# Performance work log

Hardware: AMD Instinct MI355X
Metric: run time of the kernel (lower is better)

## Reference

```python
import jax, jax.numpy as jnp
import numpy as np

N, N1, K3, K2 = 120000, 15000, 27, 8  # points at full / stride-2 resolution, kernel volumes
C, NCLS = 32, 17

relu = jax.nn.relu

def sparse_conv(x, nbr, W):
    # gather-GEMM form of sparse 3D conv: out[m] = sum_k W[k] @ x[nbr[m,k]], nbr=-1 -> inactive offset
    valid = (nbr >= 0)[..., None].astype(x.dtype)
    g = jnp.take(x, jnp.maximum(nbr, 0), axis=0) * valid  # (M, K, Cin)
    return jnp.einsum('mkc,kco->mo', g, W)

def bnorm(x, gb, eps=1e-5):
    # batch-norm over the point dim (training-mode batch statistics); gb = [gamma; beta]
    mu = x.mean(axis=0)
    var = x.var(axis=0)
    return gb[0] * (x - mu) * jax.lax.rsqrt(var + eps) + gb[1]

def mobilevit_v2_attention(x, wi, bi, wk, bk, wv, bv, wo, bo):
    # softmax over ALL points (dim 0), global context vector, as in MobileViTv2Attention.forward
    w = jax.nn.softmax(x @ wi + bi, axis=0)                  # (M, 1)
    ctx = jnp.sum(w * (x @ wk + bk), axis=0, keepdims=True)  # (1, C)
    v = (x @ wv + bv) * ctx
    return v @ wo + bo

def setup_inputs() -> dict:
    key = jax.random.key(0)
    ks = jax.random.split(key, 30)
    f = lambda i, shape, sd: jax.random.normal(ks[i], shape, jnp.float32) * sd
    gb = lambda c: jnp.stack([jnp.ones((c,), jnp.float32), jnp.zeros((c,), jnp.float32)])
    return dict(
        x=f(0, (N, 3), 1.0),
        W_stem0=f(1, (K3, 3, C), 0.1), bn_stem0=gb(C),
        W_stem1=f(2, (K3, C, C), 0.05), bn_stem1=gb(C),
        W_down=f(3, (K2, C, C), 0.05), bn_down=gb(C),
        W_res1=f(4, (K3, C, C), 0.05), bn_res1=gb(C),
        W_res2=f(5, (K3, C, C), 0.05), bn_res2=gb(C),
        att_wi=f(6, (C, 1), 0.001), att_bi=jnp.zeros((1,), jnp.float32),
        att_wk=f(7, (C, C), 0.001), att_bk=jnp.zeros((C,), jnp.float32),
        att_wv=f(8, (C, C), 0.001), att_bv=jnp.zeros((C,), jnp.float32),
        att_wo=f(9, (C, C), 0.001), att_bo=jnp.zeros((C,), jnp.float32),
        W_up=f(10, (K2, C, C), 0.05), bn_up=gb(C),
        W_fuse1=f(11, (K3, 2 * C, C), 0.05), bn_fuse1=gb(C),
        W_fuse2=f(12, (K3, C, C), 0.05), bn_fuse2=gb(C),
        W_ds=f(13, (2 * C, C), 0.05), bn_ds=gb(C),
        W_cls=f(14, (C, NCLS), 0.05), b_cls=jnp.zeros((NCLS,), jnp.float32),
        nbr0=jax.random.randint(ks[20], (N, K3), -1, N, jnp.int32),
        nbr_down=jax.random.randint(ks[21], (N1, K2), 0, N, jnp.int32),
        nbr1=jax.random.randint(ks[22], (N1, K3), -1, N1, jnp.int32),
        nbr_up=jax.random.randint(ks[23], (N, K2), -1, N1, jnp.int32),
    )

def reference(x, W_stem0, bn_stem0, W_stem1, bn_stem1, W_down, bn_down,
              W_res1, bn_res1, W_res2, bn_res2,
              att_wi, att_bi, att_wk, att_bk, att_wv, att_bv, att_wo, att_bo,
              W_up, bn_up, W_fuse1, bn_fuse1, W_fuse2, bn_fuse2, W_ds, bn_ds,
              W_cls, b_cls, nbr0, nbr_down, nbr1, nbr_up):
    # stem: conv3+BN+ReLU x2
    x0 = relu(bnorm(sparse_conv(x, nbr0, W_stem0), bn_stem0))
    x0 = relu(bnorm(sparse_conv(x0, nbr0, W_stem1), bn_stem1))
    # stage1 downsample: BasicConvolutionBlock(ks=2, stride=2) = conv+BN+ReLU
    d = relu(bnorm(sparse_conv(x0, nbr_down, W_down), bn_down))          # (N1, C)
    # ResidualBlock with MobileViTv2 attention on the conv branch, identity shortcut
    net = bnorm(sparse_conv(relu(bnorm(sparse_conv(d, nbr1, W_res1), bn_res1)), nbr1, W_res2), bn_res2)
    net = mobilevit_v2_attention(net, att_wi, att_bi, att_wk, att_bk, att_wv, att_bv, att_wo, att_bo)
    r = relu(net + d)
    # BasicDeconvolutionBlock(ks=2, stride=2): transpose conv (gather form) + BN + ReLU
    u = relu(bnorm(sparse_conv(r, nbr_up, W_up), bn_up))                 # (N, C)
    # skip concat + ResidualBlock(2C -> C) with 1x1-conv+BN downsample shortcut
    cat = jnp.concatenate([u, x0], axis=1)                               # (N, 2C)
    net2 = bnorm(sparse_conv(relu(bnorm(sparse_conv(cat, nbr0, W_fuse1), bn_fuse1)), nbr0, W_fuse2), bn_fuse2)
    ds = bnorm(cat @ W_ds, bn_ds)
    y = relu(net2 + ds)
    # classifier
    return y @ W_cls + b_cls                                             # (N, NCLS)
```

## Files before the change

kernel.cpp:

```cpp
#include <hip/hip_runtime.h>

typedef unsigned int u32;
typedef unsigned short u16;

#define NPTS 120000
#define N1PTS 15000
#define NCLSS 17
#define NSTRIPE 16

static inline int cdiv(int a, int b) { return (a + b - 1) / b; }

typedef __attribute__((ext_vector_type(8))) short bf16x8;
typedef __attribute__((ext_vector_type(4))) float f32x4;

__device__ __forceinline__ float bflo(u32 u) { return __uint_as_float(u << 16); }
__device__ __forceinline__ float bfhi(u32 u) { return __uint_as_float(u & 0xFFFF0000u); }
__device__ __forceinline__ u32 f2bf(float f) {
    u32 u = __float_as_uint(f);
    return (u + 0x7FFFu + ((u >> 16) & 1u)) >> 16;
}
__device__ __forceinline__ u32 pack2(float a, float b) { return f2bf(a) | (f2bf(b) << 16); }

__device__ __forceinline__ f32x4 mfma16(bf16x8 a, uint4 b, f32x4 c) {
    return __builtin_amdgcn_mfma_f32_16x16x32_bf16(a, __builtin_bit_cast(bf16x8, b), c, 0, 0, 0);
}

template<int K>
__global__ __launch_bounds__(256) void transpose_nbr(
    const int* __restrict__ nbr, int* __restrict__ nbrT, int M)
{
    __shared__ int tile[256][K + 1];
    int p0 = blockIdx.x * 256;
    int t = threadIdx.x;
    int np = M - p0; if (np > 256) np = 256;
    int total = np * K;
    for (int i = t; i < total; i += 256) {
        int lp = i / K, k = i - lp * K;
        tile[lp][k] = nbr[(size_t)p0 * K + i];
    }
    __syncthreads();
    if (t < np) {
#pragma unroll
        for (int k = 0; k < K; ++k)
            nbrT[(size_t)k * M + p0 + t] = tile[t][k];
    }
}

struct WbArgs {
    const float* src[8];
    uint4* dst[8];
    int CINF[8];
    int COFF[8];
    int K2[8];
};

__global__ __launch_bounds__(64) void convert_wb(WbArgs a) {
    int j = blockIdx.y;
    int s2 = blockIdx.x;
    if (s2 >= a.K2[j]) return;
    int lane = threadIdx.x;
    int k = s2 >> 1, tile = s2 & 1;
    int c = a.COFF[j] + (lane >> 4) * 8;
    int o = tile * 16 + (lane & 15);
    const float* w = a.src[j] + ((size_t)k * a.CINF[j] + c) * 32 + o;
    u32 hw[4], lw[4];
#pragma unroll
    for (int q = 0; q < 4; ++q) {
        float w0 = w[(2 * q) * 32], w1 = w[(2 * q + 1) * 32];
        u32 h0 = f2bf(w0), h1 = f2bf(w1);
        float r0 = w0 - __uint_as_float(h0 << 16);
        float r1 = w1 - __uint_as_float(h1 << 16);
        hw[q] = h0 | (h1 << 16);
        lw[q] = f2bf(r0) | (f2bf(r1) << 16);
    }
    uint4 hv; hv.x = hw[0]; hv.y = hw[1]; hv.z = hw[2]; hv.w = hw[3];
    uint4 lv; lv.x = lw[0]; lv.y = lw[1]; lv.z = lw[2]; lv.w = lw[3];
    a.dst[j][(size_t)(s2 * 2 + 0) * 64 + lane] = hv;
    a.dst[j][(size_t)(s2 * 2 + 1) * 64 + lane] = lv;
}

template<int KB, int MODE, int NPH>
__global__ __launch_bounds__(1024, 8) void conv_part(
    const u16* __restrict__ src, const int* __restrict__ nbrTk,
    const uint4* __restrict__ wb, float* __restrict__ T,
    u16* __restrict__ out, float* __restrict__ stats, int M, int Msrc)
{
    __shared__ uint4 wl[KB * 256];
    __shared__ int il[KB * 256];
    __shared__ float red[15][64];
    int tid = threadIdx.x;
    int lane = tid & 63, wid = tid >> 6;
    int p0 = blockIdx.x * 256 + wid * 16;
    int row = lane & 15, hi4 = lane >> 4;
    int lpt = wid * 16 + row;
    int col = lane & 15;
    const uint4 z4 = {0u, 0u, 0u, 0u};

    for (int i = tid; i < KB * 256; i += 1024) wl[i] = wb[i];
    for (int i = tid; i < KB * 256; i += 1024) {
        int k = i >> 8, pl = i & 255;
        int pp = blockIdx.x * 256 + pl;
        il[i] = (pp < M) ? nbrTk[(size_t)k * M + pp] : -1;
    }

    f32x4 acc0, acc1;
    if (MODE >= 1) {
#pragma unroll
        for (int r = 0; r < 4; ++r) {
            int pp = p0 + hi4 * 4 + r;
            int ps = pp < M ? pp : 0;
            acc0[r] = T[(size_t)ps * 32 + col];
            acc1[r] = T[(size_t)ps * 32 + 16 + col];
        }
    } else {
        acc0 = {0.f, 0.f, 0.f, 0.f};
        acc1 = {0.f, 0.f, 0.f, 0.f};
    }

    __syncthreads();

    const int PHSZ = (Msrc + NPH - 1) / NPH;

    auto gld = [&](int k, int lo, int hi) -> uint4 {
        int idx = il[(k << 8) + lpt];
        uint4 r = z4;
        if (idx >= lo && idx < hi)
            r = reinterpret_cast<const uint4*>(src + (size_t)idx * 32)[hi4];
        return r;
    };

#pragma unroll 1
    for (int ph = 0; ph < NPH; ++ph) {
        int lo = (NPH == 1) ? 0 : ph * PHSZ;
        int hi = (NPH == 1) ? 0x7FFFFFFF : lo + PHSZ;
        uint4 g0 = gld(0, lo, hi);
        uint4 g1 = (KB > 1) ? gld(1, lo, hi) : z4;
        uint4 g2 = (KB > 2) ? gld(2, lo, hi) : z4;
#pragma unroll 1
        for (int k = 0; k < KB; ++k) {
            uint4 gn = (k + 3 < KB) ? gld(k + 3, lo, hi) : z4;
            const uint4* bl = &wl[k * 256];
            bf16x8 a = __builtin_bit_cast(bf16x8, g0);
            acc0 = mfma16(a, bl[lane], acc0);
            acc0 = mfma16(a, bl[64 + lane], acc0);
            acc1 = mfma16(a, bl[128 + lane], acc1);
            acc1 = mfma16(a, bl[192 + lane], acc1);
            g0 = g1; g1 = g2; g2 = gn;
        }
    }

    if (MODE <= 1) {
#pragma unroll
        for (int r = 0; r < 4; ++r) {
            int pp = p0 + hi4 * 4 + r;
            if (pp < M) {
                T[(size_t)pp * 32 + col] = acc0[r];
                T[(size_t)pp * 32 + 16 + col] = acc1[r];
            }
        }
        return;
    }

#pragma unroll
    for (int r = 0; r < 4; ++r) {
        int pp = p0 + hi4 * 4 + r;
        if (pp < M) {
            out[(size_t)pp * 32 + col] = (u16)f2bf(acc0[r]);
            out[(size_t)pp * 32 + 16 + col] = (u16)f2bf(acc1[r]);
        }
    }
    float s0 = 0.f, q0 = 0.f, s1 = 0.f, q1 = 0.f;
#pragma unroll
    for (int r = 0; r < 4; ++r) {
        s0 += acc0[r]; q0 += acc0[r] * acc0[r];
        s1 += acc1[r]; q1 += acc1[r] * acc1[r];
    }
#pragma unroll
    for (int m = 16; m <= 32; m <<= 1) {
        s0 += __shfl_xor(s0, m, 64); q0 += __shfl_xor(q0, m, 64);
        s1 += __shfl_xor(s1, m, 64); q1 += __shfl_xor(q1, m, 64);
    }
    float val = (lane < 16) ? s0 : (lane < 32) ? s1 : (lane < 48) ? q0 : q1;
    if (wid > 0) red[wid - 1][lane] = val;
    __syncthreads();
    if (wid == 0) {
        float t = val;
#pragma unroll
        for (int w = 0; w < 15; ++w) t += red[w][lane];
        atomicAdd(&stats[((blockIdx.x & (NSTRIPE - 1)) << 6) + lane], t);
    }
}

__global__ __launch_bounds__(1024, 8) void conv_blk8(
    const u16* __restrict__ src, const int* __restrict__ nbrT,
    const uint4* __restrict__ wb, u16* __restrict__ out,
    float* __restrict__ stats, int M)
{
    constexpr int K = 8;
    __shared__ uint4 wl[K * 256];
    __shared__ int il[K * 256];
    __shared__ float red[15][64];
    int tid = threadIdx.x;
    int lane = tid & 63, wid = tid >> 6;
    int p0 = blockIdx.x * 256 + wid * 16;
    int row = lane & 15, hi4 = lane >> 4;
    int lpt = wid * 16 + row;
    const uint4 z4 = {0u, 0u, 0u, 0u};

    for (int i = tid; i < K * 256; i += 1024) wl[i] = wb[i];
    for (int i = tid; i < K * 256; i += 1024) {
        int k = i >> 8, pl = i & 255;
        int pp = blockIdx.x * 256 + pl;
        il[i] = (pp < M) ? nbrT[(size_t)k * M + pp] : -1;
    }

    f32x4 acc0 = {0.f, 0.f, 0.f, 0.f};
    f32x4 acc1 = {0.f, 0.f, 0.f, 0.f};

    __syncthreads();

    auto gld = [&](int k) -> uint4 {
        int idx = il[(k << 8) + lpt];
        int j = idx >= 0 ? idx : 0;
        uint4 v = reinterpret_cast<const uint4*>(src + (size_t)j * 32)[hi4];
        u32 m = (idx >= 0) ? 0xFFFFFFFFu : 0u;
        uint4 r; r.x = v.x & m; r.y = v.y & m; r.z = v.z & m; r.w = v.w & m;
        return r;
    };

    uint4 g0 = gld(0);
    uint4 g1 = gld(1);
    uint4 g2 = gld(2);

#pragma unroll 1
    for (int k = 0; k < K; ++k) {
        uint4 gn = (k + 3 < K) ? gld(k + 3) : z4;
        const uint4* bl = &wl[k * 256];
        bf16x8 a = __builtin_bit_cast(bf16x8, g0);
        acc0 = mfma16(a, bl[lane], acc0);
        acc0 = mfma16(a, bl[64 + lane], acc0);
        acc1 = mfma16(a, bl[128 + lane], acc1);
        acc1 = mfma16(a, bl[192 + lane], acc1);
        g0 = g1; g1 = g2; g2 = gn;
    }

#pragma unroll
    for (int r = 0; r < 4; ++r) {
        int pp = p0 + hi4 * 4 + r;
        if (pp < M) {
            out[(size_t)pp * 32 + (lane & 15)] = (u16)f2bf(acc0[r]);
            out[(size_t)pp * 32 + 16 + (lane & 15)] = (u16)f2bf(acc1[r]);
        }
    }

    float s0 = 0.f, q0 = 0.f, s1 = 0.f, q1 = 0.f;
#pragma unroll
    for (int r = 0; r < 4; ++r) {
        s0 += acc0[r]; q0 += acc0[r] * acc0[r];
        s1 += acc1[r]; q1 += acc1[r] * acc1[r];
    }
#pragma unroll
    for (int m = 16; m <= 32; m <<= 1) {
        s0 += __shfl_xor(s0, m, 64); q0 += __shfl_xor(q0, m, 64);
        s1 += __shfl_xor(s1, m, 64); q1 += __shfl_xor(q1, m, 64);
    }
    float val = (lane < 16) ? s0 : (lane < 32) ? s1 : (lane < 48) ? q0 : q1;
    if (wid > 0) red[wid - 1][lane] = val;
    __syncthreads();
    if (wid == 0) {
        float t = val;
#pragma unroll
        for (int w = 0; w < 15; ++w) t += red[w][lane];
        atomicAdd(&stats[((blockIdx.x & (NSTRIPE - 1)) << 6) + lane], t);
    }
}

template<int K>
__global__ __launch_bounds__(256, 6) void conv_mfma(
    const u16* __restrict__ src, const int* __restrict__ nbrT,
    const uint4* __restrict__ wb, u16* __restrict__ out,
    float* __restrict__ stats, int M)
{
    constexpr int KS = K;
    constexpr int NCH = (KS + 1) / 2;
    __shared__ uint4 wlds[2][512];
    __shared__ float red[4][64];

    int tid = threadIdx.x;
    int lane = tid & 63, wid = tid >> 6;
    int p0 = blockIdx.x * 64 + wid * 16;
    int row = lane & 15, hi4 = lane >> 4;
    int p = p0 + row;
    bool rowok = p < M;
    const uint4 z4 = {0u, 0u, 0u, 0u};

    f32x4 acc0 = {0.f, 0.f, 0.f, 0.f};
    f32x4 acc1 = {0.f, 0.f, 0.f, 0.f};

    {
        uint4 a0 = wb[tid], a1 = wb[256 + tid];
        wlds[0][tid] = a0; wlds[0][256 + tid] = a1;
    }
    uint4 av0 = z4, av1 = z4;
    {
        int iA = -1, iB = -1;
        if (rowok) {
            iA = nbrT[p];
            if (KS > 1) iB = nbrT[(size_t)M + p];
        }
        if (iA >= 0) av0 = reinterpret_cast<const uint4*>(src + (size_t)iA * 32)[hi4];
        if (KS > 1 && iB >= 0) av1 = reinterpret_cast<const uint4*>(src + (size_t)iB * 32)[hi4];
    }

    uint4 wr0 = z4, wr1 = z4;
#pragma unroll 1
    for (int c = 0; c < NCH; ++c) {
        bool last = (c + 1 >= NCH);
        if (!last) {
            wr0 = wb[(size_t)(c + 1) * 512 + tid];
            wr1 = wb[(size_t)(c + 1) * 512 + 256 + tid];
        }
        int nA = -1, nB = -1;
        if (!last && rowok) {
            int s0 = 2 * c + 2;
            nA = nbrT[(size_t)s0 * M + p];
            if (s0 + 1 < KS) nB = nbrT[(size_t)(s0 + 1) * M + p];
        }
        asm volatile("s_waitcnt lgkmcnt(0)" ::: "memory");
        __builtin_amdgcn_s_barrier();
        asm volatile("" ::: "memory");
        uint4 nav0 = z4, nav1 = z4;
        if (nA >= 0) nav0 = reinterpret_cast<const uint4*>(src + (size_t)nA * 32)[hi4];
        if (nB >= 0) nav1 = reinterpret_cast<const uint4*>(src + (size_t)nB * 32)[hi4];

        const uint4* bl = wlds[c & 1];
        {
            bf16x8 a = __builtin_bit_cast(bf16x8, av0);
            acc0 = mfma16(a, bl[lane], acc0);
            acc0 = mfma16(a, bl[64 + lane], acc0);
            acc1 = mfma16(a, bl[128 + lane], acc1);
            acc1 = mfma16(a, bl[192 + lane], acc1);
        }
        if (2 * c + 1 < KS) {
            bf16x8 a = __builtin_bit_cast(bf16x8, av1);
            acc0 = mfma16(a, bl[256 + lane], acc0);
            acc0 = mfma16(a, bl[320 + lane], acc0);
            acc1 = mfma16(a, bl[384 + lane], acc1);
            acc1 = mfma16(a, bl[448 + lane], acc1);
        }
        if (!last) {
            wlds[(c + 1) & 1][tid] = wr0;
            wlds[(c + 1) & 1][256 + tid] = wr1;
        }
        av0 = nav0; av1 = nav1;
    }

#pragma unroll
    for (int r = 0; r < 4; ++r) {
        int pp = p0 + hi4 * 4 + r;
        if (pp < M) {
            out[(size_t)pp * 32 + (lane & 15)] = (u16)f2bf(acc0[r]);
            out[(size_t)pp * 32 + 16 + (lane & 15)] = (u16)f2bf(acc1[r]);
        }
    }

    float s0 = 0.f, q0 = 0.f, s1 = 0.f, q1 = 0.f;
#pragma unroll
    for (int r = 0; r < 4; ++r) {
        s0 += acc0[r]; q0 += acc0[r] * acc0[r];
        s1 += acc1[r]; q1 += acc1[r] * acc1[r];
    }
#pragma unroll
    for (int m = 16; m <= 32; m <<= 1) {
        s0 += __shfl_xor(s0, m, 64); q0 += __shfl_xor(q0, m, 64);
        s1 += __shfl_xor(s1, m, 64); q1 += __shfl_xor(q1, m, 64);
    }
    float val = (lane < 16) ? s0 : (lane < 32) ? s1 : (lane < 48) ? q0 : q1;
    red[wid][lane] = val;
    __syncthreads();
    if (wid == 0) {
        float t = red[0][lane] + red[1][lane] + red[2][lane] + red[3][lane];
        atomicAdd(&stats[((blockIdx.x & (NSTRIPE - 1)) << 6) + lane], t);
    }
}

__device__ __forceinline__ void reduce_store_stats(
    float (&acc)[32], int lane, int wid, bool act, int p,
    u16* __restrict__ out, float* __restrict__ sst)
{
    __shared__ float lds[3][64][17];
#pragma unroll
    for (int r = 0; r < 2; ++r) {
        if (wid > 0) {
#pragma unroll
            for (int j = 0; j < 16; ++j) lds[wid - 1][lane][j] = acc[r * 16 + j];
        }
        __syncthreads();
        if (wid == 0) {
#pragma unroll
            for (int w = 0; w < 3; ++w)
#pragma unroll
                for (int j = 0; j < 16; ++j) acc[r * 16 + j] += lds[w][lane][j];
        }
        __syncthreads();
    }
    if (wid == 0) {
        if (act) {
            u32 wd[16];
#pragma unroll
            for (int q = 0; q < 16; ++q) wd[q] = pack2(acc[2 * q], acc[2 * q + 1]);
            uint4* dst = reinterpret_cast<uint4*>(out + (size_t)p * 32);
            uint4 v;
            v.x = wd[0];  v.y = wd[1];  v.z = wd[2];  v.w = wd[3];  dst[0] = v;
            v.x = wd[4];  v.y = wd[5];  v.z = wd[6];  v.w = wd[7];  dst[1] = v;
            v.x = wd[8];  v.y = wd[9];  v.z = wd[10]; v.w = wd[11]; dst[2] = v;
            v.x = wd[12]; v.y = wd[13]; v.z = wd[14]; v.w = wd[15]; dst[3] = v;
        } else {
#pragma unroll
            for (int o = 0; o < 32; ++o) acc[o] = 0.f;
        }
        float sel1 = 0.f, sel2 = 0.f;
#pragma unroll
        for (int o = 0; o < 32; ++o) {
            float s1 = acc[o], s2 = acc[o] * acc[o];
#pragma unroll
            for (int m = 1; m <= 32; m <<= 1) { s1 += __shfl_xor(s1, m, 64); s2 += __shfl_xor(s2, m, 64); }
            if (lane == o) sel1 = s1;
            if (lane == o + 32) sel2 = s2;
        }
        atomicAdd(&sst[lane], lane < 32 ? sel1 : sel2);
    }
}

__global__ __launch_bounds__(256, 8) void conv_x3(
    const float* __restrict__ src, const int* __restrict__ nbrT,
    const float* __restrict__ W, u16* __restrict__ out,
    float* __restrict__ stats, int M)
{
    constexpr int K = 27;
    int lane = threadIdx.x & 63;
    int wid = __builtin_amdgcn_readfirstlane(threadIdx.x >> 6);
    int p = blockIdx.x * 64 + lane;
    bool act = p < M;
    constexpr int JMAX = 7;

    float acc[32];
#pragma unroll
    for (int o = 0; o < 32; ++o) acc[o] = 0.f;

    int idxs[JMAX];
#pragma unroll
    for (int j = 0; j < JMAX; ++j) {
        int k = wid + 4 * j;
        idxs[j] = (act && k < K) ? nbrT[(size_t)k * M + p] : -1;
    }
#pragma unroll
    for (int j = 0; j < JMAX; ++j) {
        int k = wid + 4 * j;
        if (k >= K) break;
        int idx = idxs[j];
        if (idx >= 0) {
            const float* __restrict__ xr = src + (size_t)idx * 3;
            const float* __restrict__ wk = W + (size_t)k * 3 * 32;
            float x0 = xr[0], x1 = xr[1], x2 = xr[2];
#pragma unroll
            for (int o = 0; o < 32; ++o) {
                float s = fmaf(x0, wk[o], 0.f);
                s = fmaf(x1, wk[32 + o], s);
                acc[o] += fmaf(x2, wk[64 + o], s);
            }
        }
    }
    reduce_store_stats(acc, lane, wid, act, p, out,
                       stats + ((blockIdx.x & (NSTRIPE - 1)) << 6));
}

__global__ __launch_bounds__(256, 4) void conv_ds2(
    const u16* __restrict__ u, const u16* __restrict__ x0,
    const float* __restrict__ W, u16* __restrict__ out,
    float* __restrict__ stats, int M)
{
    int lane = threadIdx.x & 63;
    int wid = __builtin_amdgcn_readfirstlane(threadIdx.x >> 6);
    int p = blockIdx.x * 64 + lane;
    bool act = p < M;

    float acc[32];
#pragma unroll
    for (int o = 0; o < 32; ++o) acc[o] = 0.f;

    if (act) {
        const u16* srcp = (wid < 2) ? u : x0;
        const uint4* xr = reinterpret_cast<const uint4*>(srcp + (size_t)p * 32 + (wid & 1) * 16);
        const float* wk = W + (size_t)wid * 16 * 32;
#pragma unroll
        for (int h = 0; h < 2; ++h) {
            uint4 v = xr[h];
            float xv[8] = { bflo(v.x), bfhi(v.x), bflo(v.y), bfhi(v.y),
                            bflo(v.z), bfhi(v.z), bflo(v.w), bfhi(v.w) };
#pragma unroll
            for (int c = 0; c < 8; ++c)
#pragma unroll
                for (int o = 0; o < 32; ++o)
                    acc[o] = fmaf(xv[c], wk[(h * 8 + c) * 32 + o], acc[o]);
        }
    }
    reduce_store_stats(acc, lane, wid, act, p, out,
                       stats + ((blockIdx.x & (NSTRIPE - 1)) << 6));
}

template<bool RELU>
__global__ __launch_bounds__(256) void bn_apply(
    u16* __restrict__ buf, const float* __restrict__ stats,
    const float* __restrict__ gb, float invM, int total)
{
    __shared__ float ab[64];
    if (threadIdx.x < 32) {
        int c = threadIdx.x;
        float s = 0.f, q = 0.f;
#pragma unroll
        for (int st = 0; st < NSTRIPE; ++st) {
            s += stats[st * 64 + c];
            q += stats[st * 64 + 32 + c];
        }
        float mu = s * invM;
        float var = fmaxf(q * invM - mu * mu, 0.f);
        float a = gb[c] * rsqrtf(var + 1e-5f);
        ab[c] = a;
        ab[32 + c] = gb[32 + c] - mu * a;
    }
    __syncthreads();
    int i = blockIdx.x * 256 + threadIdx.x;
    if (i >= total) return;
    int c0 = (i & 3) * 8;
    uint4 v = reinterpret_cast<uint4*>(buf)[i];
    u32 w[4] = { v.x, v.y, v.z, v.w };
    u32 r[4];
#pragma unroll
    for (int q = 0; q < 4; ++q) {
        int c = c0 + 2 * q;
        float y0 = fmaf(ab[c], bflo(w[q]), ab[32 + c]);
        float y1 = fmaf(ab[c + 1], bfhi(w[q]), ab[32 + c + 1]);
        if (RELU) { y0 = fmaxf(y0, 0.f); y1 = fmaxf(y1, 0.f); }
        r[q] = pack2(y0, y1);
    }
    uint4 o; o.x = r[0]; o.y = r[1]; o.z = r[2]; o.w = r[3];
    reinterpret_cast<uint4*>(buf)[i] = o;
}

__device__ __forceinline__ void load_row32(const u16* __restrict__ base, int p, float (&nv)[32])
{
    const uint4* xr = reinterpret_cast<const uint4*>(base + (size_t)p * 32);
#pragma unroll
    for (int q = 0; q < 4; ++q) {
        uint4 v = xr[q];
        nv[q * 8 + 0] = bflo(v.x); nv[q * 8 + 1] = bfhi(v.x);
        nv[q * 8 + 2] = bflo(v.y); nv[q * 8 + 3] = bfhi(v.y);
        nv[q * 8 + 4] = bflo(v.z); nv[q * 8 + 5] = bfhi(v.z);
        nv[q * 8 + 6] = bflo(v.w); nv[q * 8 + 7] = bfhi(v.w);
    }
}

__global__ __launch_bounds__(256) void att_logits(
    const u16* __restrict__ net, const float* __restrict__ wi,
    const float* __restrict__ bi, float* __restrict__ lbuf,
    u32* __restrict__ mx, int M)
{
    int p = blockIdx.x * 256 + threadIdx.x;
    float l = -3.0e38f;
    if (p < M) {
        float nv[32];
        load_row32(net, p, nv);
        float s = bi[0];
#pragma unroll
        for (int c = 0; c < 32; ++c) s = fmaf(nv[c], wi[c], s);
        lbuf[p] = s;
        l = s;
    }
#pragma unroll
    for (int m = 1; m <= 32; m <<= 1) l = fmaxf(l, __shfl_xor(l, m, 64));
    if ((threadIdx.x & 63) == 0) {
        u32 b = __float_as_uint(l);
        u32 e = (b & 0x80000000u) ? ~b : (b | 0x80000000u);
        atomicMax(mx, e);
    }
}

__global__ __launch_bounds__(256) void att_accum(
    const u16* __restrict__ net, const float* __restrict__ lbuf,
    float* __restrict__ att, int M)
{
    int p = blockIdx.x * 256 + threadIdx.x;
    int lane = threadIdx.x & 63, wid = threadIdx.x >> 6;
    u32 um = __float_as_uint(att[0]);
    float mx = (um & 0x80000000u) ? __uint_as_float(um ^ 0x80000000u) : __uint_as_float(~um);
    float w = 0.f;
    float nv[32];
#pragma unroll
    for (int c = 0; c < 32; ++c) nv[c] = 0.f;
    if (p < M) {
        w = expf(lbuf[p] - mx);
        load_row32(net, p, nv);
    }
    float sel = 0.f;
#pragma unroll
    for (int c = 0; c < 32; ++c) {
        float s = w * nv[c];
#pragma unroll
        for (int m = 1; m <= 32; m <<= 1) s += __shfl_xor(s, m, 64);
        if (lane == c) sel = s;
    }
    {
        float s = w;
#pragma unroll
        for (int m = 1; m <= 32; m <<= 1) s += __shfl_xor(s, m, 64);
        if (lane == 32) sel = s;
    }
    __shared__ float red[4][33];
    if (lane < 33) red[wid][lane] = sel;
    __syncthreads();
    if (wid == 0 && lane < 33) {
        float t = red[0][lane] + red[1][lane] + red[2][lane] + red[3][lane];
        atomicAdd(lane < 32 ? &att[2 + lane] : &att[1], t);
    }
}

__global__ void att_ctx_k(const float* __restrict__ wk, const float* __restrict__ bk,
                          float* __restrict__ att)
{
    int o = threadIdx.x;
    if (o >= 32) return;
    float invS = 1.0f / att[1];
    float s = bk[o];
#pragma unroll
    for (int c = 0; c < 32; ++c) s = fmaf(att[2 + c] * invS, wk[c * 32 + o], s);
    att[34 + o] = s;
}

__global__ __launch_bounds__(256) void att_out_res(
    const u16* __restrict__ net, const u16* __restrict__ d,
    const float* __restrict__ wv, const float* __restrict__ bv,
    const float* __restrict__ wo, const float* __restrict__ bo,
    const float* __restrict__ att, u16* __restrict__ r, int M)
{
    int p = blockIdx.x * 256 + threadIdx.x;
    if (p >= M) return;
    float nv[32];
    load_row32(net, p, nv);
    float vv[32];
#pragma unroll
    for (int o = 0; o < 32; ++o) {
        float s = bv[o];
#pragma unroll
        for (int c = 0; c < 32; ++c) s = fmaf(nv[c], wv[c * 32 + o], s);
        vv[o] = s * att[34 + o];
    }
    float dv[32];
    load_row32(d, p, dv);
    u32 wd[16];
#pragma unroll
    for (int q = 0; q < 16; ++q) {
        float y[2];
#pragma unroll
        for (int t = 0; t < 2; ++t) {
            int oo = 2 * q + t;
            float s = bo[oo];
#pragma unroll
            for (int o = 0; o < 32; ++o) s = fmaf(vv[o], wo[o * 32 + oo], s);
            y[t] = fmaxf(s + dv[oo], 0.f);
        }
        wd[q] = pack2(y[0], y[1]);
    }
    uint4* dst = reinterpret_cast<uint4*>(r + (size_t)p * 32);
    uint4 v;
    v.x = wd[0];  v.y = wd[1];  v.z = wd[2];  v.w = wd[3];  dst[0] = v;
    v.x = wd[4];  v.y = wd[5];  v.z = wd[6];  v.w = wd[7];  dst[1] = v;
    v.x = wd[8];  v.y = wd[9];  v.z = wd[10]; v.w = wd[11]; dst[2] = v;
    v.x = wd[12]; v.y = wd[13]; v.z = wd[14]; v.w = wd[15]; dst[3] = v;
}

__global__ __launch_bounds__(256) void final_cls(
    const u16* __restrict__ net2, const u16* __restrict__ dsr,
    const float* __restrict__ st7, const float* __restrict__ st8,
    const float* __restrict__ gb7, const float* __restrict__ gb8,
    const float* __restrict__ wcls, const float* __restrict__ bcls,
    float* __restrict__ outp, float invM, int M)
{
    __shared__ float ab7[64], ab8[64];
    if (threadIdx.x < 64) {
        int c = threadIdx.x & 31;
        const float* st = (threadIdx.x < 32) ? st7 : st8;
        const float* g  = (threadIdx.x < 32) ? gb7 : gb8;
        float* abp      = (threadIdx.x < 32) ? ab7 : ab8;
        float s = 0.f, q = 0.f;
#pragma unroll
        for (int k = 0; k < NSTRIPE; ++k) {
            s += st[k * 64 + c];
            q += st[k * 64 + 32 + c];
        }
        float mu = s * invM;
        float var = fmaxf(q * invM - mu * mu, 0.f);
        float a = g[c] * rsqrtf(var + 1e-5f);
        abp[c] = a;
        abp[32 + c] = g[32 + c] - mu * a;
    }
    __syncthreads();
    int p = blockIdx.x * 256 + threadIdx.x;
    if (p >= M) return;
    float nv[32], dv[32];
    load_row32(net2, p, nv);
    load_row32(dsr, p, dv);
    float y[32];
#pragma unroll
    for (int c = 0; c < 32; ++c) {
        float t = fmaf(ab7[c], nv[c], ab7[32 + c]) + fmaf(ab8[c], dv[c], ab8[32 + c]);
        y[c] = fmaxf(t, 0.f);
    }
#pragma unroll
    for (int j = 0; j < NCLSS; ++j) {
        float s = bcls[j];
#pragma unroll
        for (int c = 0; c < 32; ++c) s = fmaf(y[c], wcls[c * NCLSS + j], s);
        outp[(size_t)p * NCLSS + j] = s;
    }
}

extern "C" void kernel_launch(void* const* d_in, const int* in_sizes, int n_in,
                              void* d_out, int out_size, void* d_ws, size_t ws_size,
                              hipStream_t stream)
{
    char* wsb = (char*)d_ws;

    float* ST  = (float*)wsb;
    float* ATT = ST + 9216;
    float* L   = (float*)(wsb + 65536);
    const size_t SZN = 7680000ull;
    const size_t SZ1 = 960000ull;
    u16* A  = (u16*)(wsb + 131072);
    u16* B  = (u16*)(wsb + 131072 + SZN);
    u16* C  = (u16*)(wsb + 131072 + 2 * SZN);
    u16* D  = (u16*)(wsb + 131072 + 2 * SZN + SZ1);
    u16* E  = (u16*)(wsb + 131072 + 2 * SZN + 2 * SZ1);
    u16* G  = (u16*)(wsb + 131072 + 2 * SZN + 3 * SZ1);
    float* T = (float*)(wsb + 131072 + 3 * SZN + 3 * SZ1);

    size_t wboff = 131072 + 3 * SZN + 3 * SZ1 + 15360000ull;
    auto wbsz = [](int K) { return (size_t)((K + 1) & ~1) * 4096; };
    uint4* wb_stem1 = (uint4*)(wsb + wboff);         size_t o1 = wboff + wbsz(27);
    uint4* wb_down  = (uint4*)(wsb + o1);            size_t o2 = o1 + wbsz(8);
    uint4* wb_res1  = (uint4*)(wsb + o2);            size_t o3 = o2 + wbsz(27);
    uint4* wb_res2  = (uint4*)(wsb + o3);            size_t o4 = o3 + wbsz(27);
    uint4* wb_up    = (uint4*)(wsb + o4);            size_t o5 = o4 + wbsz(8);
    uint4* wb_f1A   = (uint4*)(wsb + o5);            size_t o6 = o5 + wbsz(27);
    uint4* wb_f1B   = (uint4*)(wsb + o6);            size_t o7 = o6 + wbsz(27);
    uint4* wb_fuse2 = (uint4*)(wsb + o7);            size_t o8 = o7 + wbsz(27);

    int* nbrT0 = (int*)(wsb + o8);                   size_t o9  = o8 + 27ull * NPTS * 4;
    int* nbrTd = (int*)(wsb + o9);                   size_t o10 = o9 + 8ull * N1PTS * 4;
    int* nbrT1 = (int*)(wsb + o10);                  size_t o11 = o10 + 27ull * N1PTS * 4;
    int* nbrTu = (int*)(wsb + o11);

    const float* X        = (const float*)d_in[0];
    const float* Wstem0   = (const float*)d_in[1];
    const float* gb_stem0 = (const float*)d_in[2];
    const float* Wstem1   = (const float*)d_in[3];
    const float* gb_stem1 = (const float*)d_in[4];
    const float* Wdown    = (const float*)d_in[5];
    const float* gb_down  = (const float*)d_in[6];
    const float* Wres1    = (const float*)d_in[7];
    const float* gb_res1  = (const float*)d_in[8];
    const float* Wres2    = (const float*)d_in[9];
    const float* gb_res2  = (const float*)d_in[10];
    const float* wi = (const float*)d_in[11];
    const float* bi = (const float*)d_in[12];
    const float* wk = (const float*)d_in[13];
    const float* bk = (const float*)d_in[14];
    const float* wv = (const float*)d_in[15];
    const float* bv = (const float*)d_in[16];
    const float* wo = (const float*)d_in[17];
    const float* bo = (const float*)d_in[18];
    const float* Wup      = (const float*)d_in[19];
    const float* gb_up    = (const float*)d_in[20];
    const float* Wfuse1   = (const float*)d_in[21];
    const float* gb_fuse1 = (const float*)d_in[22];
    const float* Wfuse2   = (const float*)d_in[23];
    const float* gb_fuse2 = (const float*)d_in[24];
    const float* Wds      = (const float*)d_in[25];
    const float* gb_ds    = (const float*)d_in[26];
    const float* Wcls     = (const float*)d_in[27];
    const float* bcls     = (const float*)d_in[28];

    const int* nbr0     = (const int*)d_in[29];
    const int* nbr_down = (const int*)d_in[30];
    const int* nbr1     = (const int*)d_in[31];
    const int* nbr_up   = (const int*)d_in[32];

    const float invN  = 1.0f / (float)NPTS;
    const float invN1 = 1.0f / (float)N1PTS;

    hipMemsetAsync((void*)ST, 0, (9216 + 66) * sizeof(float), stream);

    hipLaunchKernelGGL((transpose_nbr<27>), dim3(cdiv(NPTS, 256)), dim3(256), 0, stream,
                       nbr0, nbrT0, NPTS);
    hipLaunchKernelGGL((transpose_nbr<8>), dim3(cdiv(N1PTS, 256)), dim3(256), 0, stream,
                       nbr_down, nbrTd, N1PTS);
    hipLaunchKernelGGL((transpose_nbr<27>), dim3(cdiv(N1PTS, 256)), dim3(256), 0, stream,
                       nbr1, nbrT1, N1PTS);
    hipLaunchKernelGGL((transpose_nbr<8>), dim3(cdiv(NPTS, 256)), dim3(256), 0, stream,
                       nbr_up, nbrTu, NPTS);

    {
        WbArgs a;
        a.src[0] = Wstem1; a.dst[0] = wb_stem1; a.CINF[0] = 32; a.COFF[0] = 0;  a.K2[0] = 54;
        a.src[1] = Wdown;  a.dst[1] = wb_down;  a.CINF[1] = 32; a.COFF[1] = 0;  a.K2[1] = 16;
        a.src[2] = Wres1;  a.dst[2] = wb_res1;  a.CINF[2] = 32; a.COFF[2] = 0;  a.K2[2] = 54;
        a.src[3] = Wres2;  a.dst[3] = wb_res2;  a.CINF[3] = 32; a.COFF[3] = 0;  a.K2[3] = 54;
        a.src[4] = Wup;    a.dst[4] = wb_up;    a.CINF[4] = 32; a.COFF[4] = 0;  a.K2[4] = 16;
        a.src[5] = Wfuse1; a.dst[5] = wb_f1A;   a.CINF[5] = 64; a.COFF[5] = 0;  a.K2[5] = 54;
        a.src[6] = Wfuse1; a.dst[6] = wb_f1B;   a.CINF[6] = 64; a.COFF[6] = 32; a.K2[6] = 54;
        a.src[7] = Wfuse2; a.dst[7] = wb_fuse2; a.CINF[7] = 32; a.COFF[7] = 0;  a.K2[7] = 54;
        hipLaunchKernelGGL(convert_wb, dim3(54, 8), dim3(64), 0, stream, a);
    }

    const int gS   = cdiv(NPTS, 64);
    const int gB   = cdiv(NPTS, 256);
    const int gM1  = cdiv(N1PTS, 64);
    const int gBN  = cdiv(NPTS * 4, 256);
    const int gBN1 = cdiv(N1PTS * 4, 256);
    const int gN1p = cdiv(N1PTS, 256);
    const int gN   = cdiv(NPTS, 256);
    const int KH0 = 14;

    hipLaunchKernelGGL(conv_x3, dim3(gS), dim3(256), 0, stream,
                       X, nbrT0, Wstem0, A, ST + 0 * 1024, NPTS);
    hipLaunchKernelGGL((bn_apply<true>), dim3(gBN), dim3(256), 0, stream,
                       A, ST + 0 * 1024, gb_stem0, invN, NPTS * 4);
    hipLaunchKernelGGL((conv_part<14, 0, 2>), dim3(gB), dim3(1024), 0, stream,
                       A, nbrT0, wb_stem1, T, (u16*)nullptr, (float*)nullptr, NPTS, NPTS);
    hipLaunchKernelGGL((conv_part<13, 2, 2>), dim3(gB), dim3(1024), 0, stream,
                       A, nbrT0 + (size_t)KH0 * NPTS, wb_stem1 + KH0 * 256, T, B, ST + 1 * 1024, NPTS, NPTS);
    hipLaunchKernelGGL((bn_apply<true>), dim3(gBN), dim3(256), 0, stream,
                       B, ST + 1 * 1024, gb_stem1, invN, NPTS * 4);

    hipLaunchKernelGGL((conv_mfma<8>), dim3(gM1), dim3(256), 0, stream,
                       B, nbrTd, wb_down, C, ST + 2 * 1024, N1PTS);
    hipLaunchKernelGGL((bn_apply<true>), dim3(gBN1), dim3(256), 0, stream,
                       C, ST + 2 * 1024, gb_down, invN1, N1PTS * 4);

    hipLaunchKernelGGL((conv_mfma<27>), dim3(gM1), dim3(256), 0, stream,
                       C, nbrT1, wb_res1, D, ST + 3 * 1024, N1PTS);
    hipLaunchKernelGGL((bn_apply<true>), dim3(gBN1), dim3(256), 0, stream,
                       D, ST + 3 * 1024, gb_res1, invN1, N1PTS * 4);
    hipLaunchKernelGGL((conv_mfma<27>), dim3(gM1), dim3(256), 0, stream,
                       D, nbrT1, wb_res2, E, ST + 4 * 1024, N1PTS);
    hipLaunchKernelGGL((bn_apply<false>), dim3(gBN1), dim3(256), 0, stream,
                       E, ST + 4 * 1024, gb_res2, invN1, N1PTS * 4);

    hipLaunchKernelGGL(att_logits, dim3(gN1p), dim3(256), 0, stream,
                       E, wi, bi, L, (u32*)ATT, N1PTS);
    hipLaunchKernelGGL(att_accum, dim3(gN1p), dim3(256), 0, stream, E, L, ATT, N1PTS);
    hipLaunchKernelGGL(att_ctx_k, dim3(1), dim3(64), 0, stream, wk, bk, ATT);
    hipLaunchKernelGGL(att_out_res, dim3(gN1p), dim3(256), 0, stream,
                       E, C, wv, bv, wo, bo, ATT, D, N1PTS);

    hipLaunchKernelGGL(conv_blk8, dim3(gB), dim3(1024), 0, stream,
                       D, nbrTu, wb_up, A, ST + 5 * 1024, NPTS);
    hipLaunchKernelGGL((bn_apply<true>), dim3(gBN), dim3(256), 0, stream,
                       A, ST + 5 * 1024, gb_up, invN, NPTS * 4);

    hipLaunchKernelGGL((conv_part<14, 0, 2>), dim3(gB), dim3(1024), 0, stream,
                       A, nbrT0, wb_f1A, T, (u16*)nullptr, (float*)nullptr, NPTS, NPTS);
    hipLaunchKernelGGL((conv_part<13, 1, 2>), dim3(gB), dim3(1024), 0, stream,
                       A, nbrT0 + (size_t)KH0 * NPTS, wb_f1A + KH0 * 256, T,
                       (u16*)nullptr, (float*)nullptr, NPTS, NPTS);
    hipLaunchKernelGGL((conv_part<14, 1, 2>), dim3(gB), dim3(1024), 0, stream,
                       B, nbrT0, wb_f1B, T, (u16*)nullptr, (float*)nullptr, NPTS, NPTS);
    hipLaunchKernelGGL(conv_ds2, dim3(gS), dim3(256), 0, stream,
                       A, B, Wds, G, ST + 8 * 1024, NPTS);
    hipLaunchKernelGGL((conv_part<13, 2, 2>), dim3(gB), dim3(1024), 0, stream,
                       B, nbrT0 + (size_t)KH0 * NPTS, wb_f1B + KH0 * 256, T, A, ST + 6 * 1024, NPTS, NPTS);
    hipLaunchKernelGGL((bn_apply<true>), dim3(gBN), dim3(256), 0, stream,
                       A, ST + 6 * 1024, gb_fuse1, invN, NPTS * 4);

    hipLaunchKernelGGL((conv_part<14, 0, 2>), dim3(gB), dim3(1024), 0, stream,
                       A, nbrT0, wb_fuse2, T, (u16*)nullptr, (float*)nullptr, NPTS, NPTS);
    hipLaunchKernelGGL((conv_part<13, 2, 2>), dim3(gB), dim3(1024), 0, stream,
                       A, nbrT0 + (size_t)KH0 * NPTS, wb_fuse2 + KH0 * 256, T, B, ST + 7 * 1024, NPTS, NPTS);

    hipLaunchKernelGGL(final_cls, dim3(gN), dim3(256), 0, stream,
                       B, G, ST + 7 * 1024, ST + 8 * 1024, gb_fuse2, gb_ds,
                       Wcls, bcls, (float*)d_out, invN, NPTS);
}
```

Before: 375.4 us.

## Fuse BN+ReLU apply into consumer conv gathers, drop standalone bn_apply passes

Result: slower. 528.4 us (+40.7%).

```diff
diff --git a/kernel.cpp b/kernel.cpp
--- a/kernel.cpp
+++ b/kernel.cpp
@@ -20,9 +20,27 @@
     return (u + 0x7FFFu + ((u >> 16) & 1u)) >> 16;
 }
 __device__ __forceinline__ u32 pack2(float a, float b) { return f2bf(a) | (f2bf(b) << 16); }
+__device__ __forceinline__ float bfround(float f) { return __uint_as_float(f2bf(f) << 16); }
 
 __device__ __forceinline__ f32x4 mfma16(bf16x8 a, uint4 b, f32x4 c) {
     return __builtin_amdgcn_mfma_f32_16x16x32_bf16(a, __builtin_bit_cast(bf16x8, b), c, 0, 0, 0);
+}
+
+__device__ __forceinline__ void stats_to_ab(
+    const float* __restrict__ bst, const float* __restrict__ bgb,
+    float binvM, int c, float* __restrict__ abl)
+{
+    float s = 0.f, q = 0.f;
+#pragma unroll
+    for (int st = 0; st < NSTRIPE; ++st) {
+        s += bst[st * 64 + c];
+        q += bst[st * 64 + 32 + c];
+    }
+    float mu = s * binvM;
+    float var = fmaxf(q * binvM - mu * mu, 0.f);
+    float a = bgb[c] * rsqrtf(var + 1e-5f);
+    abl[c] = a;
+    abl[32 + c] = bgb[32 + c] - mu * a;
 }
 
 template<int K>
@@ -79,15 +97,18 @@
     a.dst[j][(size_t)(s2 * 2 + 1) * 64 + lane] = lv;
 }
 
-template<int KB, int MODE, int NPH>
+template<int KB, int MODE, int NPH, bool BN>
 __global__ __launch_bounds__(1024, 8) void conv_part(
     const u16* __restrict__ src, const int* __restrict__ nbrTk,
     const uint4* __restrict__ wb, float* __restrict__ T,
-    u16* __restrict__ out, float* __restrict__ stats, int M, int Msrc)
+    u16* __restrict__ out, float* __restrict__ stats,
+    const float* __restrict__ bst, const float* __restrict__ bgb, float binvM,
+    int M, int Msrc)
 {
     __shared__ uint4 wl[KB * 256];
     __shared__ int il[KB * 256];
     __shared__ float red[15][64];
+    __shared__ float abl[64];
     int tid = threadIdx.x;
     int lane = tid & 63, wid = tid >> 6;
     int p0 = blockIdx.x * 256 + wid * 16;
@@ -96,6 +117,8 @@
     int col = lane & 15;
     const uint4 z4 = {0u, 0u, 0u, 0u};
 
+    if (BN && tid < 32) stats_to_ab(bst, bgb, binvM, tid, abl);
+
     for (int i = tid; i < KB * 256; i += 1024) wl[i] = wb[i];
     for (int i = tid; i < KB * 256; i += 1024) {
         int k = i >> 8, pl = i & 255;
@@ -119,13 +142,31 @@
 
     __syncthreads();
 
+    float la[8], lb[8];
+    if (BN) {
+#pragma unroll
+        for (int j = 0; j < 8; ++j) { la[j] = abl[hi4 * 8 + j]; lb[j] = abl[32 + hi4 * 8 + j]; }
+    }
+
     const int PHSZ = (Msrc + NPH - 1) / NPH;
 
     auto gld = [&](int k, int lo, int hi) -> uint4 {
         int idx = il[(k << 8) + lpt];
         uint4 r = z4;
-        if (idx >= lo && idx < hi)
-            r = reinterpret_cast<const uint4*>(src + (size_t)idx * 32)[hi4];
+        if (idx >= lo && idx < hi) {
+            uint4 v = reinterpret_cast<const uint4*>(src + (size_t)idx * 32)[hi4];
+            if (BN) {
+                u32 w[4] = { v.x, v.y, v.z, v.w };
+#pragma unroll
+                for (int q2 = 0; q2 < 4; ++q2) {
+                    float y0 = fmaxf(fmaf(la[2 * q2], bflo(w[q2]), lb[2 * q2]), 0.f);
+                    float y1 = fmaxf(fmaf(la[2 * q2 + 1], bfhi(w[q2]), lb[2 * q2 + 1]), 0.f);
+                    w[q2] = pack2(y0, y1);
+                }
+                v.x = w[0]; v.y = w[1]; v.z = w[2]; v.w = w[3];
+            }
+            r = v;
+        }
         return r;
     };
 
@@ -275,16 +316,19 @@
     }
 }
 
-template<int K>
+template<int K, bool BN>
 __global__ __launch_bounds__(256, 6) void conv_mfma(
     const u16* __restrict__ src, const int* __restrict__ nbrT,
     const uint4* __restrict__ wb, u16* __restrict__ out,
-    float* __restrict__ stats, int M)
+    float* __restrict__ stats,
+    const float* __restrict__ bst, const float* __restrict__ bgb, float binvM,
+    int M)
 {
     constexpr int KS = K;
     constexpr int NCH = (KS + 1) / 2;
     __shared__ uint4 wlds[2][512];
     __shared__ float red[4][64];
+    __shared__ float abl[64];
 
     int tid = threadIdx.x;
     int lane = tid & 63, wid = tid >> 6;
@@ -297,10 +341,31 @@
     f32x4 acc0 = {0.f, 0.f, 0.f, 0.f};
     f32x4 acc1 = {0.f, 0.f, 0.f, 0.f};
 
+    if (BN && tid < 32) stats_to_ab(bst, bgb, binvM, tid, abl);
     {
         uint4 a0 = wb[tid], a1 = wb[256 + tid];
         wlds[0][tid] = a0; wlds[0][256 + tid] = a1;
     }
+    __syncthreads();
+
+    float la[8], lb[8];
+    if (BN) {
+#pragma unroll
+        for (int j = 0; j < 8; ++j) { la[j] = abl[hi4 * 8 + j]; lb[j] = abl[32 + hi4 * 8 + j]; }
+    }
+    auto bnfix = [&](uint4 v) -> uint4 {
+        if (!BN) return v;
+        u32 w[4] = { v.x, v.y, v.z, v.w };
+#pragma unroll
+        for (int q2 = 0; q2 < 4; ++q2) {
+            float y0 = fmaxf(fmaf(la[2 * q2], bflo(w[q2]), lb[2 * q2]), 0.f);
+            float y1 = fmaxf(fmaf(la[2 * q2 + 1], bfhi(w[q2]), lb[2 * q2 + 1]), 0.f);
+            w[q2] = pack2(y0, y1);
+        }
+        uint4 r2; r2.x = w[0]; r2.y = w[1]; r2.z = w[2]; r2.w = w[3];
+        return r2;
+    };
+
     uint4 av0 = z4, av1 = z4;
     {
         int iA = -1, iB = -1;
@@ -308,8 +373,8 @@
             iA = nbrT[p];
             if (KS > 1) iB = nbrT[(size_t)M + p];
         }
-        if (iA >= 0) av0 = reinterpret_cast<const uint4*>(src + (size_t)iA * 32)[hi4];
-        if (KS > 1 && iB >= 0) av1 = reinterpret_cast<const uint4*>(src + (size_t)iB * 32)[hi4];
+        if (iA >= 0) av0 = bnfix(reinterpret_cast<const uint4*>(src + (size_t)iA * 32)[hi4]);
+        if (KS > 1 && iB >= 0) av1 = bnfix(reinterpret_cast<const uint4*>(src + (size_t)iB * 32)[hi4]);
     }
 
     uint4 wr0 = z4, wr1 = z4;
@@ -330,8 +395,8 @@
         __builtin_amdgcn_s_barrier();
         asm volatile("" ::: "memory");
         uint4 nav0 = z4, nav1 = z4;
-        if (nA >= 0) nav0 = reinterpret_cast<const uint4*>(src + (size_t)nA * 32)[hi4];
-        if (nB >= 0) nav1 = reinterpret_cast<const uint4*>(src + (size_t)nB * 32)[hi4];
+        if (nA >= 0) nav0 = bnfix(reinterpret_cast<const uint4*>(src + (size_t)nA * 32)[hi4]);
+        if (nB >= 0) nav1 = bnfix(reinterpret_cast<const uint4*>(src + (size_t)nB * 32)[hi4]);
 
         const uint4* bl = wlds[c & 1];
         {
@@ -478,16 +543,35 @@
 __global__ __launch_bounds__(256, 4) void conv_ds2(
     const u16* __restrict__ u, const u16* __restrict__ x0,
     const float* __restrict__ W, u16* __restrict__ out,
-    float* __restrict__ stats, int M)
-{
+    float* __restrict__ stats,
+    const float* __restrict__ ust, const float* __restrict__ ugb,
+    const float* __restrict__ xst, const float* __restrict__ xgb,
+    float binvM, int M)
+{
+    __shared__ float abu[64], abx[64];
     int lane = threadIdx.x & 63;
     int wid = __builtin_amdgcn_readfirstlane(threadIdx.x >> 6);
+    if (threadIdx.x < 64) {
+        int c = threadIdx.x & 31;
+        if (threadIdx.x < 32) stats_to_ab(ust, ugb, binvM, c, abu);
+        else                  stats_to_ab(xst, xgb, binvM, c, abx);
+    }
+    __syncthreads();
+
     int p = blockIdx.x * 64 + lane;
     bool act = p < M;
 
     float acc[32];
 #pragma unroll
     for (int o = 0; o < 32; ++o) acc[o] = 0.f;
+
+    const float* abp = (wid < 2) ? abu : abx;
+    float la[16], lb[16];
+#pragma unroll
+    for (int j = 0; j < 16; ++j) {
+        la[j] = abp[(wid & 1) * 16 + j];
+        lb[j] = abp[32 + (wid & 1) * 16 + j];
+    }
 
     if (act) {
         const u16* srcp = (wid < 2) ? u : x0;
@@ -499,10 +583,13 @@
             float xv[8] = { bflo(v.x), bfhi(v.x), bflo(v.y), bfhi(v.y),
                             bflo(v.z), bfhi(v.z), bflo(v.w), bfhi(v.w) };
 #pragma unroll
-            for (int c = 0; c < 8; ++c)
+            for (int c = 0; c < 8; ++c) {
+                float y = fmaxf(fmaf(la[h * 8 + c], xv[c], lb[h * 8 + c]), 0.f);
+                y = bfround(y);
 #pragma unroll
                 for (int o = 0; o < 32; ++o)
-                    acc[o] = fmaf(xv[c], wk[(h * 8 + c) * 32 + o], acc[o]);
+                    acc[o] = fmaf(y, wk[(h * 8 + c) * 32 + o], acc[o]);
+            }
         }
     }
     reduce_store_stats(acc, lane, wid, act, p, out,
@@ -515,20 +602,7 @@
     const float* __restrict__ gb, float invM, int total)
 {
     __shared__ float ab[64];
-    if (threadIdx.x < 32) {
-        int c = threadIdx.x;
-        float s = 0.f, q = 0.f;
-#pragma unroll
-        for (int st = 0; st < NSTRIPE; ++st) {
-            s += stats[st * 64 + c];
-            q += stats[st * 64 + 32 + c];
-        }
-        float mu = s * invM;
-        float var = fmaxf(q * invM - mu * mu, 0.f);
-        float a = gb[c] * rsqrtf(var + 1e-5f);
-        ab[c] = a;
-        ab[32 + c] = gb[32 + c] - mu * a;
-    }
+    if (threadIdx.x < 32) stats_to_ab(stats, gb, invM, threadIdx.x, ab);
     __syncthreads();
     int i = blockIdx.x * 256 + threadIdx.x;
     if (i >= total) return;
@@ -638,11 +712,15 @@
 }
 
 __global__ __launch_bounds__(256) void att_out_res(
-    const u16* __restrict__ net, const u16* __restrict__ d,
+    const u16* __restrict__ net, const u16* __restrict__ draw,
     const float* __restrict__ wv, const float* __restrict__ bv,
     const float* __restrict__ wo, const float* __restrict__ bo,
-    const float* __restrict__ att, u16* __restrict__ r, int M)
-{
+    const float* __restrict__ att, u16* __restrict__ r,
+    const float* __restrict__ dst_, const float* __restrict__ dgb, float dinvM, int M)
+{
+    __shared__ float abd[64];
+    if (threadIdx.x < 32) stats_to_ab(dst_, dgb, dinvM, threadIdx.x, abd);
+    __syncthreads();
     int p = blockIdx.x * 256 + threadIdx.x;
     if (p >= M) return;
     float nv[32];
@@ -656,7 +734,10 @@
         vv[o] = s * att[34 + o];
     }
     float dv[32];
-    load_row32(d, p, dv);
+    load_row32(draw, p, dv);
+#pragma unroll
+    for (int c = 0; c < 32; ++c)
+        dv[c] = bfround(fmaxf(fmaf(abd[c], dv[c], abd[32 + c]), 0.f));
     u32 wd[16];
 #pragma unroll
     for (int q = 0; q < 16; ++q) {
@@ -689,20 +770,8 @@
     __shared__ float ab7[64], ab8[64];
     if (threadIdx.x < 64) {
         int c = threadIdx.x & 31;
-        const float* st = (threadIdx.x < 32) ? st7 : st8;
-        const float* g  = (threadIdx.x < 32) ? gb7 : gb8;
-        float* abp      = (threadIdx.x < 32) ? ab7 : ab8;
-        float s = 0.f, q = 0.f;
-#pragma unroll
-        for (int k = 0; k < NSTRIPE; ++k) {
-            s += st[k * 64 + c];
-            q += st[k * 64 + 32 + c];
-        }
-        float mu = s * invM;
-        float var = fmaxf(q * invM - mu * mu, 0.f);
-        float a = g[c] * rsqrtf(var + 1e-5f);
-        abp[c] = a;
-        abp[32 + c] = g[32 + c] - mu * a;
+        if (threadIdx.x < 32) stats_to_ab(st7, gb7, invM, c, ab7);
+        else                  stats_to_ab(st8, gb8, invM, c, ab8);
     }
     __syncthreads();
     int p = blockIdx.x * 256 + threadIdx.x;
@@ -825,69 +894,72 @@
     const int gS   = cdiv(NPTS, 64);
     const int gB   = cdiv(NPTS, 256);
     const int gM1  = cdiv(N1PTS, 64);
-    const int gBN  = cdiv(NPTS * 4, 256);
     const int gBN1 = cdiv(N1PTS * 4, 256);
     const int gN1p = cdiv(N1PTS, 256);
     const int gN   = cdiv(NPTS, 256);
     const int KH0 = 14;
 
+    float* st0 = ST + 0 * 1024;
+    float* st1 = ST + 1 * 1024;
+    float* st2 = ST + 2 * 1024;
+    float* st3 = ST + 3 * 1024;
+    float* st4 = ST + 4 * 1024;
+    float* st5 = ST + 5 * 1024;
+    float* st6 = ST + 6 * 1024;
+    float* st7 = ST + 7 * 1024;
+    float* st8 = ST + 8 * 1024;
+
     hipLaunchKernelGGL(conv_x3, dim3(gS), dim3(256), 0, stream,
-                       X, nbrT0, Wstem0, A, ST + 0 * 1024, NPTS);
-    hipLaunchKernelGGL((bn_apply<true>), dim3(gBN), dim3(256), 0, stream,
-                       A, ST + 0 * 1024, gb_stem0, invN, NPTS * 4);
-    hipLaunchKernelGGL((conv_part<14, 0, 2>), dim3(gB), dim3(1024), 0, stream,
-                       A, nbrT0, wb_stem1, T, (u16*)nullptr, (float*)nullptr, NPTS, NPTS);
-    hipLaunchKernelGGL((conv_part<13, 2, 2>), dim3(gB), dim3(1024), 0, stream,
-                       A, nbrT0 + (size_t)KH0 * NPTS, wb_stem1 + KH0 * 256, T, B, ST + 1 * 1024, NPTS, NPTS);
-    hipLaunchKernelGGL((bn_apply<true>), dim3(gBN), dim3(256), 0, stream,
-                       B, ST + 1 * 1024, gb_stem1, invN, NPTS * 4);
-
-    hipLaunchKernelGGL((conv_mfma<8>), dim3(gM1), dim3(256), 0, stream,
-                       B, nbrTd, wb_down, C, ST + 2 * 1024, N1PTS);
-    hipLaunchKernelGGL((bn_apply<true>), dim3(gBN1), dim3(256), 0, stream,
-                       C, ST + 2 * 1024, gb_down, invN1, N1PTS * 4);
-
-    hipLaunchKernelGGL((conv_mfma<27>), dim3(gM1), dim3(256), 0, stream,
-                       C, nbrT1, wb_res1, D, ST + 3 * 1024, N1PTS);
-    hipLaunchKernelGGL((bn_apply<true>), dim3(gBN1), dim3(256), 0, stream,
-                       D, ST + 3 * 1024, gb_res1, invN1, N1PTS * 4);
-    hipLaunchKernelGGL((conv_mfma<27>), dim3(gM1), dim3(256), 0, stream,
-                       D, nbrT1, wb_res2, E, ST + 4 * 1024, N1PTS);
+                       X, nbrT0, Wstem0, A, st0, NPTS);
+    hipLaunchKernelGGL((conv_part<14, 0, 2, true>), dim3(gB), dim3(1024), 0, stream,
+                       A, nbrT0, wb_stem1, T, (u16*)nullptr, (float*)nullptr,
+                       st0, gb_stem0, invN, NPTS, NPTS);
+    hipLaunchKernelGGL((conv_part<13, 2, 2, true>), dim3(gB), dim3(1024), 0, stream,
+                       A, nbrT0 + (size_t)KH0 * NPTS, wb_stem1 + KH0 * 256, T, B, st1,
+                       st0, gb_stem0, invN, NPTS, NPTS);
+
+    hipLaunchKernelGGL((conv_mfma<8, true>), dim3(gM1), dim3(256), 0, stream,
+                       B, nbrTd, wb_down, C, st2, st1, gb_stem1, invN, N1PTS);
+    hipLaunchKernelGGL((conv_mfma<27, true>), dim3(gM1), dim3(256), 0, stream,
+                       C, nbrT1, wb_res1, D, st3, st2, gb_down, invN1, N1PTS);
+    hipLaunchKernelGGL((conv_mfma<27, true>), dim3(gM1), dim3(256), 0, stream,
+                       D, nbrT1, wb_res2, E, st4, st3, gb_res1, invN1, N1PTS);
     hipLaunchKernelGGL((bn_apply<false>), dim3(gBN1), dim3(256), 0, stream,
-                       E, ST + 4 * 1024, gb_res2, invN1, N1PTS * 4);
+                       E, st4, gb_res2, invN1, N1PTS * 4);
 
     hipLaunchKernelGGL(att_logits, dim3(gN1p), dim3(256), 0, stream,
                        E, wi, bi, L, (u32*)ATT, N1PTS);
     hipLaunchKernelGGL(att_accum, dim3(gN1p), dim3(256), 0, stream, E, L, ATT, N1PTS);
     hipLaunchKernelGGL(att_ctx_k, dim3(1), dim3(64), 0, stream, wk, bk, ATT);
     hipLaunchKernelGGL(att_out_res, dim3(gN1p), dim3(256), 0, stream,
-                       E, C, wv, bv, wo, bo, ATT, D, N1PTS);
+                       E, C, wv, bv, wo, bo, ATT, D, st2, gb_down, invN1, N1PTS);
 
     hipLaunchKernelGGL(conv_blk8, dim3(gB), dim3(1024), 0, stream,
-                       D, nbrTu, wb_up, A, ST + 5 * 1024, NPTS);
-    hipLaunchKernelGGL((bn_apply<true>), dim3(gBN), dim3(256), 0, stream,
-                       A, ST + 5 * 1024, gb_up, invN, NPTS * 4);
-
-    hipLaunchKernelGGL((conv_part<14, 0, 2>), dim3(gB), dim3(1024), 0, stream,
-                       A, nbrT0, wb_f1A, T, (u16*)nullptr, (float*)nullptr, NPTS, NPTS);
-    hipLaunchKernelGGL((conv_part<13, 1, 2>), dim3(gB), dim3(1024), 0, stream,
+                       D, nbrTu, wb_up, A, st5, NPTS);
+
+    hipLaunchKernelGGL((conv_part<14, 0, 2, true>), dim3(gB), dim3(1024), 0, stream,
+                       A, nbrT0, wb_f1A, T, (u16*)nullptr, (float*)nullptr,
+                       st5, gb_up, invN, NPTS, NPTS);
+    hipLaunchKernelGGL((conv_part<13, 1, 2, true>), dim3(gB), dim3(1024), 0, stream,
                        A, nbrT0 + (size_t)KH0 * NPTS, wb_f1A + KH0 * 256, T,
-                       (u16*)nullptr, (float*)nullptr, NPTS, NPTS);
-    hipLaunchKernelGGL((conv_part<14, 1, 2>), dim3(gB), dim3(1024), 0, stream,
-                       B, nbrT0, wb_f1B, T, (u16*)nullptr, (float*)nullptr, NPTS, NPTS);
+                       (u16*)nullptr, (float*)nullptr, st5, gb_up, invN, NPTS, NPTS);
+    hipLaunchKernelGGL((conv_part<14, 1, 2, true>), dim3(gB), dim3(1024), 0, stream,
+                       B, nbrT0, wb_f1B, T, (u16*)nullptr, (float*)nullptr,
+                       st1, gb_stem1, invN, NPTS, NPTS);
     hipLaunchKernelGGL(conv_ds2, dim3(gS), dim3(256), 0, stream,
-                       A, B, Wds, G, ST + 8 * 1024, NPTS);
-    hipLaunchKernelGGL((conv_part<13, 2, 2>), dim3(gB), dim3(1024), 0, stream,
-                       B, nbrT0 + (size_t)KH0 * NPTS, wb_f1B + KH0 * 256, T, A, ST + 6 * 1024, NPTS, NPTS);
-    hipLaunchKernelGGL((bn_apply<true>), dim3(gBN), dim3(256), 0, stream,
-                       A, ST + 6 * 1024, gb_fuse1, invN, NPTS * 4);
-
-    hipLaunchKernelGGL((conv_part<14, 0, 2>), dim3(gB), dim3(1024), 0, stream,
-                       A, nbrT0, wb_fuse2, T, (u16*)nullptr, (float*)nullptr, NPTS, NPTS);
-    hipLaunchKernelGGL((conv_part<13, 2, 2>), dim3(gB), dim3(1024), 0, stream,
-                       A, nbrT0 + (size_t)KH0 * NPTS, wb_fuse2 + KH0 * 256, T, B, ST + 7 * 1024, NPTS, NPTS);
+                       A, B, Wds, G, st8, st5, gb_up, st1, gb_stem1, invN, NPTS);
+    hipLaunchKernelGGL((conv_part<13, 2, 2, true>), dim3(gB), dim3(1024), 0, stream,
+                       B, nbrT0 + (size_t)KH0 * NPTS, wb_f1B + KH0 * 256, T, A, st6,
+                       st1, gb_stem1, invN, NPTS, NPTS);
+
+    hipLaunchKernelGGL((conv_part<14, 0, 2, true>), dim3(gB), dim3(1024), 0, stream,
+                       A, nbrT0, wb_fuse2, T, (u16*)nullptr, (float*)nullptr,
+                       st6, gb_fuse1, invN, NPTS, NPTS);
+    hipLaunchKernelGGL((conv_part<13, 2, 2, true>), dim3(gB), dim3(1024), 0, stream,
+                       A, nbrT0 + (size_t)KH0 * NPTS, wb_fuse2 + KH0 * 256, T, B, st7,
+                       st6, gb_fuse1, invN, NPTS, NPTS);
 
     hipLaunchKernelGGL(final_cls, dim3(gN), dim3(256), 0, stream,
-                       B, G, ST + 7 * 1024, ST + 8 * 1024, gb_fuse2, gb_ds,
+                       B, G, st7, st8, gb_fuse2, gb_ds,
                        Wcls, bcls, (float*)d_out, invN, NPTS);
 }
```
